# Performance work log

Hardware: AMD Instinct MI355X
Metric: run time of the kernel (lower is better)

The kernel has to match this reference:

```python
import jax, jax.numpy as jnp
import numpy as np

C0 = 1000  # adaptive softmax shortlist size; clusters: [1000,3000), [3000,10000), [10000,n)
SLM_LOGITS_SCALE = 0.1
BN_EPS = 1e-5
S_SENSES = 117660
V_LEMMAS = 180000
K_NNZ = 8


def _init_weights(key):
    ks = jax.random.split(key, 32)
    w = lambda i, shape: (jax.random.normal(ks[i], shape, dtype=jnp.float32) * 0.02)
    return w


def setup_inputs() -> dict:
    key = jax.random.key(0)
    w = _init_weights(key)
    inp = {
        "cached_embeddings": jax.random.normal(jax.random.fold_in(key, 100), (8, 64, 1024), dtype=jnp.float32),
        "bn_gamma": jnp.ones((1024,), jnp.float32),
        "bn_beta": jnp.zeros((1024,), jnp.float32),
        "dense_w": w(0, (512, 1024)), "dense_b": jnp.zeros((512,), jnp.float32),
        "h1_w": w(1, (512, 512)), "h1_b": jnp.zeros((512,), jnp.float32),
        "h2_w": w(2, (512, 512)), "h2_b": jnp.zeros((512,), jnp.float32),
        # WSD adaptive softmax (n_classes = 117660)
        "wsd_head_w": w(3, (C0 + 3, 512)),
        "wsd_t1_w1": w(4, (128, 512)), "wsd_t1_w2": w(5, (2000, 128)),
        "wsd_t2_w1": w(6, (32, 512)), "wsd_t2_w2": w(7, (7000, 32)),
        "wsd_t3_w1": w(8, (8, 512)), "wsd_t3_w2": w(9, (S_SENSES - 10000, 8)),
        # SLM adaptive softmax (n_classes = 180000)
        "slm_head_w": w(10, (C0 + 3, 512)),
        "slm_t1_w1": w(11, (128, 512)), "slm_t1_w2": w(12, (2000, 128)),
        "slm_t2_w1": w(13, (32, 512)), "slm_t2_w2": w(14, (7000, 32)),
        "slm_t3_w1": w(15, (8, 512)), "slm_t3_w2": w(16, (V_LEMMAS - 10000, 8)),
        # sparse sense->lemma matrix: K entries per sense row, value 1/K
        "sv_vals": jnp.full((S_SENSES, K_NNZ), 1.0 / K_NNZ, dtype=jnp.float32),
        "sv_cols": jax.random.randint(jax.random.fold_in(key, 101), (S_SENSES, K_NNZ), 0, V_LEMMAS, dtype=jnp.int32),
    }
    return inp


def ada_log_prob(h, head_w, tails):
    """PyTorch AdaptiveLogSoftmaxWithLoss.log_prob: full [N, n_classes] log-probs."""
    head_lp = jax.nn.log_softmax(h @ head_w.T, axis=-1)  # [N, C0+3]
    parts = [head_lp[:, :C0]]
    for i, (w1, w2) in enumerate(tails):
        cluster_lp = jax.nn.log_softmax((h @ w1.T) @ w2.T, axis=-1)
        parts.append(cluster_lp + head_lp[:, C0 + i][:, None])
    return jnp.concatenate(parts, axis=-1)


def reference(cached_embeddings, bn_gamma, bn_beta, dense_w, dense_b, h1_w, h1_b,
              h2_w, h2_b, wsd_head_w, wsd_t1_w1, wsd_t1_w2, wsd_t2_w1, wsd_t2_w2,
              wsd_t3_w1, wsd_t3_w2, slm_head_w, slm_t1_w1, slm_t1_w2, slm_t2_w1,
              slm_t2_w2, slm_t3_w1, slm_t3_w2, sv_vals, sv_cols):
    B, T, D = cached_embeddings.shape
    x = cached_embeddings.reshape(B * T, D)
    # batch norm (batch statistics, learned affine)
    mu = jnp.mean(x, axis=0)
    var = jnp.var(x, axis=0)
    x = (x - mu) * jax.lax.rsqrt(var + BN_EPS) * bn_gamma + bn_beta
    # dense MLP
    x = x @ dense_w.T + dense_b
    x = jax.nn.relu(x @ h1_w.T + h1_b)
    h = x @ h2_w.T + h2_b  # [N, 512]
    # SLM adaptive log-softmax over lemma vocab
    v = ada_log_prob(h, slm_head_w, [(slm_t1_w1, slm_t1_w2), (slm_t2_w1, slm_t2_w2), (slm_t3_w1, slm_t3_w2)])  # [N, V]
    # sparse.mm(sv, v.T).T : slm[n, s] = sum_k sv_vals[s,k] * v[n, sv_cols[s,k]]
    slm = v[:, sv_cols[:, 0]] * sv_vals[None, :, 0]
    for k in range(1, sv_cols.shape[1]):
        slm = slm + v[:, sv_cols[:, k]] * sv_vals[None, :, k]
    # WSD adaptive log-softmax over senses
    y = ada_log_prob(h, wsd_head_w, [(wsd_t1_w1, wsd_t1_w2), (wsd_t2_w1, wsd_t2_w2), (wsd_t3_w1, wsd_t3_w2)])  # [N, S]
    return y + slm * SLM_LOGITS_SCALE
```

## Files before the change

kernel.cpp:

```cpp
#include <hip/hip_runtime.h>
#include <stdint.h>

#define N_ROWS 512
#define D_IN 1024
#define ZCAT_COLS 2342
#define S_TOT 117660
#define S_PAD 117760
#define J_SLM 170000
#define J_WSD 107660

#define C8f  (-18.49f)
#define C17f (-18.95f)
#define C18f (-6.91f)
#define C19f (-14.51f)
#define C20f (-15.76f)
#define C21f (-6.91f)
#define C22f (-14.51f)
#define C23f (-15.76f)

typedef __attribute__((ext_vector_type(8))) short short8;
typedef __attribute__((ext_vector_type(4))) float f32x4;

__device__ inline unsigned short f2bf(float f){
  unsigned int u = __float_as_uint(f);
  u += 0x7FFF + ((u >> 16) & 1);
  return (unsigned short)(u >> 16);
}

__global__ void bn_partial(const float* __restrict__ x, float* __restrict__ colacc){
  int r0 = blockIdx.x * 8;
  int t = threadIdx.x;
  #pragma unroll
  for (int q = 0; q < 4; q++){
    int j = t + q * 256;
    float s1 = 0.f, s2 = 0.f;
    #pragma unroll
    for (int r = 0; r < 8; r++){
      float v = x[(size_t)(r0 + r) * D_IN + j];
      s1 += v; s2 += v * v;
    }
    atomicAdd(&colacc[j], s1);
    atomicAdd(&colacc[1024 + j], s2);
  }
}

__global__ void convert_all(
  const float* __restrict__ x, const float* __restrict__ colacc,
  const float* __restrict__ gamma, const float* __restrict__ beta, unsigned short* __restrict__ xbn,
  const float* __restrict__ dw, unsigned short* __restrict__ dwb,
  const float* __restrict__ h1w, unsigned short* __restrict__ h1b,
  const float* __restrict__ h2w, unsigned short* __restrict__ h2b,
  const float* __restrict__ sh, const float* __restrict__ wh,
  const float* __restrict__ s11, const float* __restrict__ w11,
  const float* __restrict__ s21, const float* __restrict__ w21,
  const float* __restrict__ s31, const float* __restrict__ w31, unsigned short* __restrict__ wcat,
  const float* __restrict__ st1w2, unsigned short* __restrict__ st1b,
  const float* __restrict__ wt1w2, unsigned short* __restrict__ wt1b,
  const float* __restrict__ st2w2, unsigned short* __restrict__ st2b,
  const float* __restrict__ wt2w2, unsigned short* __restrict__ wt2b)
{
  size_t i = (size_t)blockIdx.x * 256 + threadIdx.x;
  const size_t o1 = 524288, o2 = o1 + 524288, o3 = o2 + 262144, o4 = o3 + 262144,
               o5 = o4 + 1199104, o6 = o5 + 256000, o7 = o6 + 256000, o8 = o7 + 224000,
               o9 = o8 + 224000;
  if (i < o1){
    int c = (int)(i & 1023);
    float mu = colacc[c] * (1.0f / 512.0f);
    float var = colacc[1024 + c] * (1.0f / 512.0f) - mu * mu;
    float sc = rsqrtf(var + 1e-5f) * gamma[c];
    float shv = beta[c] - mu * sc;
    xbn[i] = f2bf(x[i] * sc + shv);
  }
  else if (i < o2){ size_t l = i - o1; dwb[l] = f2bf(dw[l]); }
  else if (i < o3){ size_t l = i - o2; h1b[l] = f2bf(h1w[l]); }
  else if (i < o4){ size_t l = i - o3; h2b[l] = f2bf(h2w[l]); }
  else if (i < o5){
    size_t l = i - o4;
    float v;
    if (l < 513536) v = sh[l];
    else if (l < 1027072) v = wh[l - 513536];
    else if (l < 1092608) v = s11[l - 1027072];
    else if (l < 1158144) v = w11[l - 1092608];
    else if (l < 1174528) v = s21[l - 1158144];
    else if (l < 1190912) v = w21[l - 1174528];
    else if (l < 1195008) v = s31[l - 1190912];
    else v = w31[l - 1195008];
    wcat[l] = f2bf(v);
  }
  else if (i < o6){ size_t l = i - o5; st1b[l] = f2bf(st1w2[l]); }
  else if (i < o7){ size_t l = i - o6; wt1b[l] = f2bf(wt1w2[l]); }
  else if (i < o8){ size_t l = i - o7; st2b[l] = f2bf(st2w2[l]); }
  else if (i < o9){ size_t l = i - o8; wt2b[l] = f2bf(wt2w2[l]); }
}

__global__ __launch_bounds__(256) void gemm_mlp(
  const unsigned short* __restrict__ A, int lda, const unsigned short* __restrict__ B,
  const float* __restrict__ bias, unsigned short* __restrict__ outB,
  int N, int K, int relu)
{
  int t = threadIdx.x; int wave = t >> 6; int L = t & 63; int quad = L >> 4; int l16 = L & 15;
  int mbase = blockIdx.y * 64 + wave * 16;
  int nb0 = blockIdx.x * 64;
  f32x4 acc[4] = {{0,0,0,0},{0,0,0,0},{0,0,0,0},{0,0,0,0}};
  int mrow = mbase + l16;
  const unsigned short* Ap = A + (size_t)mrow * lda + quad * 8;
  const unsigned short* Bp[4];
  #pragma unroll
  for (int j = 0; j < 4; j++){
    int n = nb0 + j * 16 + l16;
    if (n > N - 1) n = N - 1;
    Bp[j] = B + (size_t)n * K + quad * 8;
  }
  for (int k0 = 0; k0 < K; k0 += 32){
    short8 a = *(const short8*)(Ap + k0);
    #pragma unroll
    for (int j = 0; j < 4; j++){
      short8 b = *(const short8*)(Bp[j] + k0);
      acc[j] = __builtin_amdgcn_mfma_f32_16x16x32_bf16(a, b, acc[j], 0, 0, 0);
    }
  }
  #pragma unroll
  for (int j = 0; j < 4; j++){
    int n = nb0 + j * 16 + l16;
    if (n < N){
      float bv = bias ? bias[n] : 0.0f;
      #pragma unroll
      for (int r = 0; r < 4; r++){
        int m = mbase + quad * 4 + r;
        float v = acc[j][r] + bv;
        if (relu) v = fmaxf(v, 0.0f);
        outB[(size_t)m * N + n] = f2bf(v);
      }
    }
  }
}

__global__ __launch_bounds__(256) void gemm_zcat(
  const unsigned short* __restrict__ A, const unsigned short* __restrict__ B,
  float* __restrict__ Zcat, unsigned short* __restrict__ htcat, float* __restrict__ sums6)
{
  const int N = ZCAT_COLS, K = 512;
  int t = threadIdx.x; int wave = t >> 6; int L = t & 63; int quad = L >> 4; int l16 = L & 15;
  int mbase = blockIdx.y * 64 + wave * 16;
  int nb0 = blockIdx.x * 64;
  f32x4 acc[4] = {{0,0,0,0},{0,0,0,0},{0,0,0,0},{0,0,0,0}};
  int mrow = mbase + l16;
  const unsigned short* Ap = A + (size_t)mrow * 512 + quad * 8;
  const unsigned short* Bp[4];
  #pragma unroll
  for (int j = 0; j < 4; j++){
    int n = nb0 + j * 16 + l16;
    if (n > N - 1) n = N - 1;
    Bp[j] = B + (size_t)n * K + quad * 8;
  }
  for (int k0 = 0; k0 < K; k0 += 32){
    short8 a = *(const short8*)(Ap + k0);
    #pragma unroll
    for (int j = 0; j < 4; j++){
      short8 b = *(const short8*)(Bp[j] + k0);
      acc[j] = __builtin_amdgcn_mfma_f32_16x16x32_bf16(a, b, acc[j], 0, 0, 0);
    }
  }
  bool doEps = (nb0 < 2006);
  __shared__ float sacc[64][2];
  if (doEps){
    for (int e = threadIdx.x; e < 128; e += 256) ((float*)sacc)[e] = 0.f;
    __syncthreads();
  }
  #pragma unroll
  for (int j = 0; j < 4; j++){
    int c = nb0 + j * 16 + l16;
    #pragma unroll
    for (int r = 0; r < 4; r++){
      int m = mbase + quad * 4 + r;
      float v = acc[j][r];
      if (c < N){
        Zcat[(size_t)m * ZCAT_COLS + c] = v;
        if (c >= 2006) htcat[(size_t)m * 336 + (c - 2006)] = f2bf(v);
      }
      if (doEps){
        float e0 = (c < 1003) ? __expf(v) : 0.f;
        float e1 = (c >= 1003 && c < 2006) ? __expf(v) : 0.f;
        #pragma unroll
        for (int d = 8; d > 0; d >>= 1){ e0 += __shfl_xor(e0, d); e1 += __shfl_xor(e1, d); }
        if (l16 == 0){
          int mr = wave * 16 + quad * 4 + r;
          if (e0 != 0.f) atomicAdd(&sacc[mr][0], e0);
          if (e1 != 0.f) atomicAdd(&sacc[mr][1], e1);
        }
      }
    }
  }
  if (doEps){
    __syncthreads();
    int tt = threadIdx.x;
    if (tt < 128){
      int mr = tt >> 1;
      float v = sacc[mr][tt & 1];
      if (v != 0.f) atomicAdd(&sums6[(blockIdx.y * 64 + mr) * 8 + (tt & 1)], v);
    }
  }
}

__global__ __launch_bounds__(256) void gemm_tail(
  const unsigned short* __restrict__ htcat,
  const unsigned short* __restrict__ b0, const unsigned short* __restrict__ b1,
  const unsigned short* __restrict__ b2, const unsigned short* __restrict__ b3,
  float* __restrict__ o0, float* __restrict__ o1, float* __restrict__ o2, float* __restrict__ o3,
  float* __restrict__ sums6)
{
  int zi = blockIdx.z;
  int N = (zi < 2) ? 2000 : 7000;
  int K = (zi < 2) ? 128 : 32;
  int aoff = (zi == 0) ? 0 : (zi == 1) ? 128 : (zi == 2) ? 256 : 288;
  const unsigned short* B = (zi == 0) ? b0 : (zi == 1) ? b1 : (zi == 2) ? b2 : b3;
  float* outF = (zi == 0) ? o0 : (zi == 1) ? o1 : (zi == 2) ? o2 : o3;
  int nb0 = blockIdx.x * 64;
  if (nb0 >= N) return;
  int t = threadIdx.x; int wave = t >> 6; int L = t & 63; int quad = L >> 4; int l16 = L & 15;
  int mbase = blockIdx.y * 64 + wave * 16;
  f32x4 acc[4] = {{0,0,0,0},{0,0,0,0},{0,0,0,0},{0,0,0,0}};
  int mrow = mbase + l16;
  const unsigned short* Ap = htcat + (size_t)mrow * 336 + aoff + quad * 8;
  const unsigned short* Bp[4];
  #pragma unroll
  for (int j = 0; j < 4; j++){
    int n = nb0 + j * 16 + l16;
    if (n > N - 1) n = N - 1;
    Bp[j] = B + (size_t)n * K + quad * 8;
  }
  for (int k0 = 0; k0 < K; k0 += 32){
    short8 a = *(const short8*)(Ap + k0);
    #pragma unroll
    for (int j = 0; j < 4; j++){
      short8 b = *(const short8*)(Bp[j] + k0);
      acc[j] = __builtin_amdgcn_mfma_f32_16x16x32_bf16(a, b, acc[j], 0, 0, 0);
    }
  }
  __shared__ float sacc[64];
  for (int e = threadIdx.x; e < 64; e += 256) sacc[e] = 0.f;
  __syncthreads();
  #pragma unroll
  for (int j = 0; j < 4; j++){
    int n = nb0 + j * 16 + l16;
    #pragma unroll
    for (int r = 0; r < 4; r++){
      int m = mbase + quad * 4 + r;
      float v = acc[j][r];
      if (n < N) outF[(size_t)m * N + n] = v;
      float e = (n < N) ? __expf(v) : 0.f;
      #pragma unroll
      for (int d = 8; d > 0; d >>= 1) e += __shfl_xor(e, d);
      if (l16 == 0) atomicAdd(&sacc[wave * 16 + quad * 4 + r], e);
    }
  }
  __syncthreads();
  if (threadIdx.x < 64){
    float v = sacc[threadIdx.x];
    atomicAdd(&sums6[(blockIdx.y * 64 + threadIdx.x) * 8 + 2 + zi], v);
  }
}

__global__ void moments_kernel(const float* __restrict__ wS, const float* __restrict__ wW,
                               float* __restrict__ mom){
  int side = blockIdx.y;
  const float* w2 = side ? wW : wS;
  int J = side ? J_WSD : J_SLM;
  float* outp = mom + side * 72;
  float s1[8]; float m2[64];
  #pragma unroll
  for (int e = 0; e < 8; e++) s1[e] = 0.f;
  #pragma unroll
  for (int e = 0; e < 64; e++) m2[e] = 0.f;
  for (int r = blockIdx.x * 256 + threadIdx.x; r < J; r += gridDim.x * 256){
    const f32x4* p = (const f32x4*)(w2 + (size_t)r * 8);
    f32x4 wa = p[0], wb = p[1];
    float w[8] = {wa[0], wa[1], wa[2], wa[3], wb[0], wb[1], wb[2], wb[3]};
    #pragma unroll
    for (int a = 0; a < 8; a++){
      s1[a] += w[a];
      #pragma unroll
      for (int b = 0; b < 8; b++) m2[a * 8 + b] += w[a] * w[b];
    }
  }
  __shared__ float lds[4][72];
  int L = threadIdx.x & 63; int wave = threadIdx.x >> 6;
  #pragma unroll
  for (int e = 0; e < 72; e++){
    float v = (e < 8) ? s1[e] : m2[e - 8];
    #pragma unroll
    for (int d = 32; d > 0; d >>= 1) v += __shfl_down(v, d);
    if (L == 0) lds[wave][e] = v;
  }
  __syncthreads();
  int tt = threadIdx.x;
  if (tt < 72){
    float v = lds[0][tt] + lds[1][tt] + lds[2][tt] + lds[3][tt];
    atomicAdd(&outp[tt], v);
  }
}

__global__ __launch_bounds__(256) void build_smallT(const float* __restrict__ Zcat,
                                                    const float* __restrict__ z1S,
                                                    const float* __restrict__ z2S,
                                                    const float* __restrict__ z1W,
                                                    const float* __restrict__ z2W,
                                                    float* __restrict__ smallT,
                                                    const float* __restrict__ sums6,
                                                    const float* __restrict__ mom,
                                                    unsigned short* __restrict__ rbf){
  int side = blockIdx.z;
  if (side == 2){
    if (blockIdx.x != 0 || blockIdx.y != 0) return;
    for (int n = threadIdx.x; n < 512; n += 256){
      const float* zrow = Zcat + (size_t)n * ZCAT_COLS;
      float lseHS = __logf(sums6[n * 8 + 0]), lseHW = __logf(sums6[n * 8 + 1]);
      float lse1S = __logf(sums6[n * 8 + 2]), lse1W = __logf(sums6[n * 8 + 3]);
      float lse2S = __logf(sums6[n * 8 + 4]), lse2W = __logf(sums6[n * 8 + 5]);
      float uS[8], uW[8];
      #pragma unroll
      for (int j = 0; j < 8; j++){ uS[j] = zrow[2326 + j]; uW[j] = zrow[2334 + j]; }
      const float* mS = mom; const float* mW = mom + 72;
      float d1 = 0.f, d2 = 0.f, e1 = 0.f, e2 = 0.f;
      #pragma unroll
      for (int a = 0; a < 8; a++){
        d1 += uS[a] * mS[a]; e1 += uW[a] * mW[a];
        #pragma unroll
        for (int b = 0; b < 8; b++){
          d2 += uS[a] * uS[b] * mS[8 + a * 8 + b];
          e2 += uW[a] * uW[b] * mW[8 + a * 8 + b];
        }
      }
      float lse3S = __logf((float)J_SLM + d1 + 0.5f * d2);
      float lse3W = __logf((float)J_WSD + e1 + 0.5f * e2);
      float C3w = (zrow[2005] - lseHW) - lse3W;
      float C3s = (zrow[1002] - lseHS) - lse3S;
      float A1s = zrow[1000] - lseHS - lse1S;
      float A2s = zrow[1001] - lseHS - lse2S;
      float A1w = zrow[2003] - lseHW - lse1W;
      float A2w = zrow[2004] - lseHW - lse2W;
      unsigned short* rr = rbf + n * 32;
      #pragma unroll
      for (int j = 0; j < 8; j++){ rr[j] = f2bf(uW[j]); rr[9 + j] = f2bf(uS[j]); }
      rr[8]  = f2bf(C3w - C8f);
      rr[17] = f2bf(C3s - C17f);
      rr[18] = f2bf(-lseHS - C18f);
      rr[19] = f2bf(A1s - C19f);
      rr[20] = f2bf(A2s - C20f);
      rr[21] = f2bf(-lseHW - C21f);
      rr[22] = f2bf(A1w - C22f);
      rr[23] = f2bf(A2w - C23f);
      #pragma unroll
      for (int j = 24; j < 32; j++) rr[j] = 0;
    }
    return;
  }
  __shared__ float tile[64][65];
  int c0 = blockIdx.x * 64, n0 = blockIdx.y * 64;
  int tlo = threadIdx.x & 63, thi = threadIdx.x >> 6;
  const float* zz1 = side ? z1W : z1S;
  const float* zz2 = side ? z2W : z2S;
  int hoff = side ? 1003 : 0;
  #pragma unroll
  for (int p = 0; p < 16; p++){
    int nl = thi + p * 4;
    int c = c0 + tlo;
    float v = 0.f;
    if (c < 1000) v = Zcat[(size_t)(n0 + nl) * ZCAT_COLS + hoff + c];
    else if (c < 3000) v = zz1[(size_t)(n0 + nl) * 2000 + (c - 1000)];
    else if (c < 10000) v = zz2[(size_t)(n0 + nl) * 7000 + (c - 3000)];
    tile[tlo][nl] = v;
  }
  __syncthreads();
  #pragma unroll
  for (int p = 0; p < 16; p++){
    int cl = thi + p * 4;
    int c = c0 + cl;
    if (c < 10000) smallT[(size_t)(side * 10000 + c) * 512 + n0 + tlo] = tile[cl][tlo];
  }
}

__global__ __launch_bounds__(256) void build_q(
  const int* __restrict__ sv_cols, const float* __restrict__ sv_vals,
  const float* __restrict__ w2S, const float* __restrict__ w2W,
  unsigned short* __restrict__ qbf, float* __restrict__ EP, int* __restrict__ nsm,
  uint2* __restrict__ cv)
{
  int s = blockIdx.x * 256 + threadIdx.x;
  if (s >= S_PAD) return;
  unsigned short qr[32];
  #pragma unroll
  for (int e = 0; e < 32; e++) qr[e] = 0;
  uint2 pairs[10];
  #pragma unroll
  for (int e = 0; e < 10; e++){ pairs[e].x = 0; pairs[e].y = 0; }
  int idx = 0; float cw = 0.f, vh = 0.f, v1s = 0.f, v2s = 0.f;
  float w8[8];
  #pragma unroll
  for (int e = 0; e < 8; e++) w8[e] = 0.f;
  if (s < S_TOT){
    if (s < 10000){ pairs[0].x = (unsigned)(10000 + s); pairs[0].y = __float_as_uint(1.0f); idx = 1; }
    #pragma unroll
    for (int k = 0; k < 8; k++){
      int c = sv_cols[(size_t)s * 8 + k];
      float v = 0.1f * sv_vals[(size_t)s * 8 + k];
      if (c >= 10000){
        cw += v;
        const float* wr = w2S + (size_t)(c - 10000) * 8;
        #pragma unroll
        for (int j = 0; j < 8; j++) w8[j] += v * wr[j];
      } else {
        pairs[idx].x = (unsigned)c; pairs[idx].y = __float_as_uint(v); idx++;
        if (c < 1000) vh += v; else if (c < 3000) v1s += v; else v2s += v;
      }
    }
    if (s >= 10000){
      const float* wrw = w2W + (size_t)(s - 10000) * 8;
      #pragma unroll
      for (int j = 0; j < 8; j++) qr[j] = f2bf(wrw[j]);
      qr[8] = f2bf(1.0f);
    }
    #pragma unroll
    for (int j = 0; j < 8; j++) qr[9 + j] = f2bf(w8[j]);
    qr[17] = f2bf(cw); qr[18] = f2bf(vh); qr[19] = f2bf(v1s); qr[20] = f2bf(v2s);
    qr[21] = f2bf(s < 1000 ? 1.f : 0.f);
    qr[22] = f2bf((s >= 1000 && s < 3000) ? 1.f : 0.f);
    qr[23] = f2bf((s >= 3000 && s < 10000) ? 1.f : 0.f);
    float ep = (s >= 10000) ? C8f : (s < 1000 ? C21f : (s < 3000 ? C22f : C23f));
    ep += cw * C17f + vh * C18f + v1s * C19f + v2s * C20f;
    EP[s] = ep;
  } else {
    EP[s] = 0.f;
  }
  nsm[s] = idx;
  #pragma unroll
  for (int e = 0; e < 10; e++) cv[(size_t)s * 10 + e] = pairs[e];
  short8* qp = (short8*)(qbf + (size_t)s * 32);
  const short8* src = (const short8*)qr;
  qp[0] = src[0]; qp[1] = src[1]; qp[2] = src[2]; qp[3] = src[3];
}

__global__ __launch_bounds__(256, 4) void final2(
  const unsigned short* __restrict__ rbf, const unsigned short* __restrict__ qbf,
  const float* __restrict__ EP, const int* __restrict__ nsm,
  const uint2* __restrict__ cv, const float* __restrict__ smallT,
  float* __restrict__ out)
{
  int t = threadIdx.x; int wave = t >> 6; int L = t & 63; int quad = L >> 4; int l16 = L & 15;
  int sbase = blockIdx.y * 256 + wave * 64;
  int nbase = blockIdx.x * 64;
  short8 bfrag[4]; float ep[4]; int cnt[4]; int kmax[4];
  int ccol[4][3]; float cval[4][3];
  #pragma unroll
  for (int j = 0; j < 4; j++){
    int s = sbase + j * 16 + l16;
    bfrag[j] = *(const short8*)(qbf + (size_t)s * 32 + quad * 8);
    ep[j] = EP[s]; cnt[j] = nsm[s];
    #pragma unroll
    for (int k = 0; k < 3; k++){
      uint2 e = cv[(size_t)s * 10 + k];
      ccol[j][k] = (int)e.x; cval[j][k] = __uint_as_float(e.y);
    }
    int kw = cnt[j];
    #pragma unroll
    for (int d = 32; d > 0; d >>= 1){ int o = __shfl_xor(kw, d); kw = (o > kw) ? o : kw; }
    kmax[j] = __builtin_amdgcn_readfirstlane(kw);
  }
  for (int i = 0; i < 4; i++){
    int n0 = nbase + i * 16;
    short8 afrag = *(const short8*)(rbf + (size_t)(n0 + l16) * 32 + quad * 8);
    int nq = n0 + quad * 4;
    #pragma unroll
    for (int j = 0; j < 4; j++){
      f32x4 acc = {0.f, 0.f, 0.f, 0.f};
      acc = __builtin_amdgcn_mfma_f32_16x16x32_bf16(afrag, bfrag[j], acc, 0, 0, 0);
      f32x4 res = acc + ep[j];
      #pragma unroll
      for (int k = 0; k < 3; k++){
        if (k < kmax[j]){
          if (k < cnt[j]){
            const f32x4* p = (const f32x4*)(smallT + ((size_t)ccol[j][k] << 9) + nq);
            res += cval[j][k] * (*p);
          }
        }
      }
      if (kmax[j] >= 4){
        int s = sbase + j * 16 + l16;
        for (int k = 3; k < 9; k++){
          if (k < cnt[j]){
            uint2 e = cv[(size_t)s * 10 + k];
            const f32x4* p = (const f32x4*)(smallT + ((size_t)e.x << 9) + nq);
            res += __uint_as_float(e.y) * (*p);
          }
        }
      }
      int sj = sbase + j * 16 + l16;
      if (sj < S_TOT){
        #pragma unroll
        for (int r = 0; r < 4; r++)
          out[(size_t)(nq + r) * S_TOT + sj] = res[r];
      }
    }
  }
}

extern "C" void kernel_launch(void* const* d_in, const int* in_sizes, int n_in,
                              void* d_out, int out_size, void* d_ws, size_t ws_size,
                              hipStream_t stream)
{
  const float* x      = (const float*)d_in[0];
  const float* gamma  = (const float*)d_in[1];
  const float* beta   = (const float*)d_in[2];
  const float* dw     = (const float*)d_in[3];
  const float* db     = (const float*)d_in[4];
  const float* h1w    = (const float*)d_in[5];
  const float* h1bias = (const float*)d_in[6];
  const float* h2w    = (const float*)d_in[7];
  const float* h2bias = (const float*)d_in[8];
  const float* whead  = (const float*)d_in[9];
  const float* wt1w1  = (const float*)d_in[10];
  const float* wt1w2  = (const float*)d_in[11];
  const float* wt2w1  = (const float*)d_in[12];
  const float* wt2w2  = (const float*)d_in[13];
  const float* wt3w1  = (const float*)d_in[14];
  const float* wt3w2  = (const float*)d_in[15];
  const float* shead  = (const float*)d_in[16];
  const float* st1w1  = (const float*)d_in[17];
  const float* st1w2  = (const float*)d_in[18];
  const float* st2w1  = (const float*)d_in[19];
  const float* st2w2  = (const float*)d_in[20];
  const float* st3w1  = (const float*)d_in[21];
  const float* st3w2  = (const float*)d_in[22];
  const float* svv    = (const float*)d_in[23];
  const int*   svc    = (const int*)d_in[24];
  float* out = (float*)d_out;

  char* wsb = (char*)d_ws; size_t off = 0;
  auto alloc = [&](size_t bytes) -> void* {
    void* p = wsb + off;
    off = (off + bytes + 255) & ~(size_t)255;
    return p;
  };
  float* colacc = (float*)alloc(2048 * 4);
  float* mom    = (float*)alloc(2 * 72 * 4);
  float* sums6  = (float*)alloc(512 * 8 * 4);
  size_t zero_bytes = ((char*)sums6 - (char*)colacc) + 512 * 8 * 4;

  unsigned short* xbn   = (unsigned short*)alloc((size_t)512 * 1024 * 2);
  unsigned short* dwb   = (unsigned short*)alloc((size_t)512 * 1024 * 2);
  unsigned short* h1b   = (unsigned short*)alloc((size_t)512 * 512 * 2);
  unsigned short* h2b   = (unsigned short*)alloc((size_t)512 * 512 * 2);
  unsigned short* wcat  = (unsigned short*)alloc((size_t)ZCAT_COLS * 512 * 2);
  unsigned short* st1b  = (unsigned short*)alloc((size_t)2000 * 128 * 2);
  unsigned short* wt1b  = (unsigned short*)alloc((size_t)2000 * 128 * 2);
  unsigned short* st2b  = (unsigned short*)alloc((size_t)7000 * 32 * 2);
  unsigned short* wt2b  = (unsigned short*)alloc((size_t)7000 * 32 * 2);
  unsigned short* a_bf  = (unsigned short*)alloc((size_t)512 * 512 * 2);
  unsigned short* t_bf  = (unsigned short*)alloc((size_t)512 * 512 * 2);
  unsigned short* h_bf  = (unsigned short*)alloc((size_t)512 * 512 * 2);
  unsigned short* htcat = (unsigned short*)alloc((size_t)512 * 336 * 2);
  float* Zcat  = (float*)alloc((size_t)512 * ZCAT_COLS * 4);
  float* z1S   = (float*)alloc((size_t)512 * 2000 * 4);
  float* z1W   = (float*)alloc((size_t)512 * 2000 * 4);
  float* z2S   = (float*)alloc((size_t)512 * 7000 * 4);
  float* z2W   = (float*)alloc((size_t)512 * 7000 * 4);
  unsigned short* rbf = (unsigned short*)alloc((size_t)512 * 32 * 2);
  float* smallT = (float*)alloc((size_t)20000 * 512 * 4);
  unsigned short* qbf = (unsigned short*)alloc((size_t)S_PAD * 32 * 2);
  float* EP  = (float*)alloc((size_t)S_PAD * 4);
  int*   nsm = (int*)alloc((size_t)S_PAD * 4);
  uint2* cv  = (uint2*)alloc((size_t)S_PAD * 10 * 8);

  (void)in_sizes; (void)n_in; (void)out_size; (void)ws_size;

  hipMemsetAsync(colacc, 0, zero_bytes, stream);
  bn_partial<<<64, 256, 0, stream>>>(x, colacc);
  convert_all<<<14578, 256, 0, stream>>>(
      x, colacc, gamma, beta, xbn, dw, dwb, h1w, h1b, h2w, h2b,
      shead, whead, st1w1, wt1w1, st2w1, wt2w1, st3w1, wt3w1, wcat,
      st1w2, st1b, wt1w2, wt1b, st2w2, st2b, wt2w2, wt2b);
  moments_kernel<<<dim3(32, 2), 256, 0, stream>>>(st3w2, wt3w2, mom);
  build_q<<<S_PAD / 256, 256, 0, stream>>>(svc, svv, st3w2, wt3w2, qbf, EP, nsm, cv);

  gemm_mlp<<<dim3(8, 8), 256, 0, stream>>>(xbn, 1024, dwb, db, a_bf, 512, 1024, 0);
  gemm_mlp<<<dim3(8, 8), 256, 0, stream>>>(a_bf, 512, h1b, h1bias, t_bf, 512, 512, 1);
  gemm_mlp<<<dim3(8, 8), 256, 0, stream>>>(t_bf, 512, h2b, h2bias, h_bf, 512, 512, 0);
  gemm_zcat<<<dim3(37, 8), 256, 0, stream>>>(h_bf, wcat, Zcat, htcat, sums6);
  gemm_tail<<<dim3(110, 8, 4), 256, 0, stream>>>(htcat, st1b, wt1b, st2b, wt2b,
                                                 z1S, z1W, z2S, z2W, sums6);
  build_smallT<<<dim3(157, 8, 3), 256, 0, stream>>>(Zcat, z1S, z2S, z1W, z2W, smallT,
                                                    sums6, mom, rbf);
  final2<<<dim3(8, 460), 256, 0, stream>>>(rbf, qbf, EP, nsm, cv, smallT, out);
}
```

Before: 617.0 us.

## Write tail GEMM outputs transposed into smallT and narrow MLP/zcat GEMM tiles

The tail GEMM now transposes its output tile through shared memory and writes straight into the smallT buffer. This removes the z1/z2 intermediate buffers and the extra pass in build_smallT that re-read and transposed them, so build_smallT shrinks to handling only the head columns. Separately, the MLP and zcat GEMMs switch from 64-wide to 16-wide N tiles per block, launching four times as many blocks for better occupancy on these small GEMMs. The narrower tiles give up B-operand reuse within a block.

```diff
diff --git a/kernel.cpp b/kernel.cpp
--- a/kernel.cpp
+++ b/kernel.cpp
@@ -100,37 +100,27 @@
 {
   int t = threadIdx.x; int wave = t >> 6; int L = t & 63; int quad = L >> 4; int l16 = L & 15;
   int mbase = blockIdx.y * 64 + wave * 16;
-  int nb0 = blockIdx.x * 64;
-  f32x4 acc[4] = {{0,0,0,0},{0,0,0,0},{0,0,0,0},{0,0,0,0}};
+  int nb0 = blockIdx.x * 16;
+  f32x4 acc = {0,0,0,0};
   int mrow = mbase + l16;
   const unsigned short* Ap = A + (size_t)mrow * lda + quad * 8;
-  const unsigned short* Bp[4];
-  #pragma unroll
-  for (int j = 0; j < 4; j++){
-    int n = nb0 + j * 16 + l16;
-    if (n > N - 1) n = N - 1;
-    Bp[j] = B + (size_t)n * K + quad * 8;
-  }
+  int nn = nb0 + l16;
+  if (nn > N - 1) nn = N - 1;
+  const unsigned short* Bp = B + (size_t)nn * K + quad * 8;
   for (int k0 = 0; k0 < K; k0 += 32){
     short8 a = *(const short8*)(Ap + k0);
-    #pragma unroll
-    for (int j = 0; j < 4; j++){
-      short8 b = *(const short8*)(Bp[j] + k0);
-      acc[j] = __builtin_amdgcn_mfma_f32_16x16x32_bf16(a, b, acc[j], 0, 0, 0);
-    }
-  }
-  #pragma unroll
-  for (int j = 0; j < 4; j++){
-    int n = nb0 + j * 16 + l16;
-    if (n < N){
-      float bv = bias ? bias[n] : 0.0f;
-      #pragma unroll
-      for (int r = 0; r < 4; r++){
-        int m = mbase + quad * 4 + r;
-        float v = acc[j][r] + bv;
-        if (relu) v = fmaxf(v, 0.0f);
-        outB[(size_t)m * N + n] = f2bf(v);
-      }
+    short8 b = *(const short8*)(Bp + k0);
+    acc = __builtin_amdgcn_mfma_f32_16x16x32_bf16(a, b, acc, 0, 0, 0);
+  }
+  int n = nb0 + l16;
+  if (n < N){
+    float bv = bias ? bias[n] : 0.0f;
+    #pragma unroll
+    for (int r = 0; r < 4; r++){
+      int m = mbase + quad * 4 + r;
+      float v = acc[r] + bv;
+      if (relu) v = fmaxf(v, 0.0f);
+      outB[(size_t)m * N + n] = f2bf(v);
     }
   }
 }
@@ -142,24 +132,17 @@
   const int N = ZCAT_COLS, K = 512;
   int t = threadIdx.x; int wave = t >> 6; int L = t & 63; int quad = L >> 4; int l16 = L & 15;
   int mbase = blockIdx.y * 64 + wave * 16;
-  int nb0 = blockIdx.x * 64;
-  f32x4 acc[4] = {{0,0,0,0},{0,0,0,0},{0,0,0,0},{0,0,0,0}};
+  int nb0 = blockIdx.x * 16;
+  f32x4 acc = {0,0,0,0};
   int mrow = mbase + l16;
   const unsigned short* Ap = A + (size_t)mrow * 512 + quad * 8;
-  const unsigned short* Bp[4];
-  #pragma unroll
-  for (int j = 0; j < 4; j++){
-    int n = nb0 + j * 16 + l16;
-    if (n > N - 1) n = N - 1;
-    Bp[j] = B + (size_t)n * K + quad * 8;
-  }
+  int nn = nb0 + l16;
+  if (nn > N - 1) nn = N - 1;
+  const unsigned short* Bp = B + (size_t)nn * K + quad * 8;
   for (int k0 = 0; k0 < K; k0 += 32){
     short8 a = *(const short8*)(Ap + k0);
-    #pragma unroll
-    for (int j = 0; j < 4; j++){
-      short8 b = *(const short8*)(Bp[j] + k0);
-      acc[j] = __builtin_amdgcn_mfma_f32_16x16x32_bf16(a, b, acc[j], 0, 0, 0);
-    }
+    short8 b = *(const short8*)(Bp + k0);
+    acc = __builtin_amdgcn_mfma_f32_16x16x32_bf16(a, b, acc, 0, 0, 0);
   }
   bool doEps = (nb0 < 2006);
   __shared__ float sacc[64][2];
@@ -167,27 +150,24 @@
     for (int e = threadIdx.x; e < 128; e += 256) ((float*)sacc)[e] = 0.f;
     __syncthreads();
   }
-  #pragma unroll
-  for (int j = 0; j < 4; j++){
-    int c = nb0 + j * 16 + l16;
-    #pragma unroll
-    for (int r = 0; r < 4; r++){
-      int m = mbase + quad * 4 + r;
-      float v = acc[j][r];
-      if (c < N){
-        Zcat[(size_t)m * ZCAT_COLS + c] = v;
-        if (c >= 2006) htcat[(size_t)m * 336 + (c - 2006)] = f2bf(v);
-      }
-      if (doEps){
-        float e0 = (c < 1003) ? __expf(v) : 0.f;
-        float e1 = (c >= 1003 && c < 2006) ? __expf(v) : 0.f;
-        #pragma unroll
-        for (int d = 8; d > 0; d >>= 1){ e0 += __shfl_xor(e0, d); e1 += __shfl_xor(e1, d); }
-        if (l16 == 0){
-          int mr = wave * 16 + quad * 4 + r;
-          if (e0 != 0.f) atomicAdd(&sacc[mr][0], e0);
-          if (e1 != 0.f) atomicAdd(&sacc[mr][1], e1);
-        }
+  int c = nb0 + l16;
+  #pragma unroll
+  for (int r = 0; r < 4; r++){
+    int m = mbase + quad * 4 + r;
+    float v = acc[r];
+    if (c < N){
+      Zcat[(size_t)m * ZCAT_COLS + c] = v;
+      if (c >= 2006) htcat[(size_t)m * 336 + (c - 2006)] = f2bf(v);
+    }
+    if (doEps){
+      float e0 = (c < 1003) ? __expf(v) : 0.f;
+      float e1 = (c >= 1003 && c < 2006) ? __expf(v) : 0.f;
+      #pragma unroll
+      for (int d = 8; d > 0; d >>= 1){ e0 += __shfl_xor(e0, d); e1 += __shfl_xor(e1, d); }
+      if (l16 == 0){
+        int mr = wave * 16 + quad * 4 + r;
+        if (e0 != 0.f) atomicAdd(&sacc[mr][0], e0);
+        if (e1 != 0.f) atomicAdd(&sacc[mr][1], e1);
       }
     }
   }
@@ -206,15 +186,14 @@
   const unsigned short* __restrict__ htcat,
   const unsigned short* __restrict__ b0, const unsigned short* __restrict__ b1,
   const unsigned short* __restrict__ b2, const unsigned short* __restrict__ b3,
-  float* __restrict__ o0, float* __restrict__ o1, float* __restrict__ o2, float* __restrict__ o3,
-  float* __restrict__ sums6)
+  float* __restrict__ smallT, float* __restrict__ sums6)
 {
   int zi = blockIdx.z;
   int N = (zi < 2) ? 2000 : 7000;
   int K = (zi < 2) ? 128 : 32;
   int aoff = (zi == 0) ? 0 : (zi == 1) ? 128 : (zi == 2) ? 256 : 288;
+  int rowbase = (zi == 0) ? 1000 : (zi == 1) ? 11000 : (zi == 2) ? 3000 : 13000;
   const unsigned short* B = (zi == 0) ? b0 : (zi == 1) ? b1 : (zi == 2) ? b2 : b3;
-  float* outF = (zi == 0) ? o0 : (zi == 1) ? o1 : (zi == 2) ? o2 : o3;
   int nb0 = blockIdx.x * 64;
   if (nb0 >= N) return;
   int t = threadIdx.x; int wave = t >> 6; int L = t & 63; int quad = L >> 4; int l16 = L & 15;
@@ -238,6 +217,7 @@
     }
   }
   __shared__ float sacc[64];
+  __shared__ float tile[64][65];
   for (int e = threadIdx.x; e < 64; e += 256) sacc[e] = 0.f;
   __syncthreads();
   #pragma unroll
@@ -245,16 +225,24 @@
     int n = nb0 + j * 16 + l16;
     #pragma unroll
     for (int r = 0; r < 4; r++){
-      int m = mbase + quad * 4 + r;
+      int mloc = wave * 16 + quad * 4 + r;
       float v = acc[j][r];
-      if (n < N) outF[(size_t)m * N + n] = v;
+      tile[j * 16 + l16][mloc] = v;
       float e = (n < N) ? __expf(v) : 0.f;
       #pragma unroll
       for (int d = 8; d > 0; d >>= 1) e += __shfl_xor(e, d);
-      if (l16 == 0) atomicAdd(&sacc[wave * 16 + quad * 4 + r], e);
+      if (l16 == 0) atomicAdd(&sacc[mloc], e);
     }
   }
   __syncthreads();
+  int tlo = t & 63, thi = t >> 6;
+  int m0 = blockIdx.y * 64 + tlo;
+  #pragma unroll
+  for (int p = 0; p < 16; p++){
+    int cl = thi + p * 4;
+    int cg = nb0 + cl;
+    if (cg < N) smallT[(size_t)(rowbase + cg) * 512 + m0] = tile[cl][tlo];
+  }
   if (threadIdx.x < 64){
     float v = sacc[threadIdx.x];
     atomicAdd(&sums6[(blockIdx.y * 64 + threadIdx.x) * 8 + 2 + zi], v);
@@ -301,10 +289,6 @@
 }
 
 __global__ __launch_bounds__(256) void build_smallT(const float* __restrict__ Zcat,
-                                                    const float* __restrict__ z1S,
-                                                    const float* __restrict__ z2S,
-                                                    const float* __restrict__ z1W,
-                                                    const float* __restrict__ z2W,
                                                     float* __restrict__ smallT,
                                                     const float* __restrict__ sums6,
                                                     const float* __restrict__ mom,
@@ -358,8 +342,6 @@
   __shared__ float tile[64][65];
   int c0 = blockIdx.x * 64, n0 = blockIdx.y * 64;
   int tlo = threadIdx.x & 63, thi = threadIdx.x >> 6;
-  const float* zz1 = side ? z1W : z1S;
-  const float* zz2 = side ? z2W : z2S;
   int hoff = side ? 1003 : 0;
   #pragma unroll
   for (int p = 0; p < 16; p++){
@@ -367,8 +349,6 @@
     int c = c0 + tlo;
     float v = 0.f;
     if (c < 1000) v = Zcat[(size_t)(n0 + nl) * ZCAT_COLS + hoff + c];
-    else if (c < 3000) v = zz1[(size_t)(n0 + nl) * 2000 + (c - 1000)];
-    else if (c < 10000) v = zz2[(size_t)(n0 + nl) * 7000 + (c - 3000)];
     tile[tlo][nl] = v;
   }
   __syncthreads();
@@ -376,7 +356,7 @@
   for (int p = 0; p < 16; p++){
     int cl = thi + p * 4;
     int c = c0 + cl;
-    if (c < 10000) smallT[(size_t)(side * 10000 + c) * 512 + n0 + tlo] = tile[cl][tlo];
+    if (c < 1000) smallT[(size_t)(side * 10000 + c) * 512 + n0 + tlo] = tile[cl][tlo];
   }
 }
 
@@ -560,10 +540,6 @@
   unsigned short* h_bf  = (unsigned short*)alloc((size_t)512 * 512 * 2);
   unsigned short* htcat = (unsigned short*)alloc((size_t)512 * 336 * 2);
   float* Zcat  = (float*)alloc((size_t)512 * ZCAT_COLS * 4);
-  float* z1S   = (float*)alloc((size_t)512 * 2000 * 4);
-  float* z1W   = (float*)alloc((size_t)512 * 2000 * 4);
-  float* z2S   = (float*)alloc((size_t)512 * 7000 * 4);
-  float* z2W   = (float*)alloc((size_t)512 * 7000 * 4);
   unsigned short* rbf = (unsigned short*)alloc((size_t)512 * 32 * 2);
   float* smallT = (float*)alloc((size_t)20000 * 512 * 4);
   unsigned short* qbf = (unsigned short*)alloc((size_t)S_PAD * 32 * 2);
@@ -582,13 +558,12 @@
   moments_kernel<<<dim3(32, 2), 256, 0, stream>>>(st3w2, wt3w2, mom);
   build_q<<<S_PAD / 256, 256, 0, stream>>>(svc, svv, st3w2, wt3w2, qbf, EP, nsm, cv);
 
-  gemm_mlp<<<dim3(8, 8), 256, 0, stream>>>(xbn, 1024, dwb, db, a_bf, 512, 1024, 0);
-  gemm_mlp<<<dim3(8, 8), 256, 0, stream>>>(a_bf, 512, h1b, h1bias, t_bf, 512, 512, 1);
-  gemm_mlp<<<dim3(8, 8), 256, 0, stream>>>(t_bf, 512, h2b, h2bias, h_bf, 512, 512, 0);
-  gemm_zcat<<<dim3(37, 8), 256, 0, stream>>>(h_bf, wcat, Zcat, htcat, sums6);
+  gemm_mlp<<<dim3(32, 8), 256, 0, stream>>>(xbn, 1024, dwb, db, a_bf, 512, 1024, 0);
+  gemm_mlp<<<dim3(32, 8), 256, 0, stream>>>(a_bf, 512, h1b, h1bias, t_bf, 512, 512, 1);
+  gemm_mlp<<<dim3(32, 8), 256, 0, stream>>>(t_bf, 512, h2b, h2bias, h_bf, 512, 512, 0);
+  gemm_zcat<<<dim3(147, 8), 256, 0, stream>>>(h_bf, wcat, Zcat, htcat, sums6);
   gemm_tail<<<dim3(110, 8, 4), 256, 0, stream>>>(htcat, st1b, wt1b, st2b, wt2b,
-                                                 z1S, z1W, z2S, z2W, sums6);
-  build_smallT<<<dim3(157, 8, 3), 256, 0, stream>>>(Zcat, z1S, z2S, z1W, z2W, smallT,
-                                                    sums6, mom, rbf);
+                                                 smallT, sums6);
+  build_smallT<<<dim3(16, 8, 3), 256, 0, stream>>>(Zcat, smallT, sums6, mom, rbf);
   final2<<<dim3(8, 460), 256, 0, stream>>>(rbf, qbf, EP, nsm, cv, smallT, out);
 }
```

After: 573.6 us. 1.08x faster.
